# Kernel tuning notes

Measured on AMD Instinct MI355X. Metric: run time of the kernel, lower is better.

## Reference

```python
import jax, jax.numpy as jnp
import numpy as np
from jax import lax

NDF = 128
OUT_CH = 256
N_INPUT = 4096
H = W = 64
A_FEAT = OUT_CH * 2 * 2   # 1024
B_OUT = OUT_CH            # 256
C_ROW = 16
BATCH = 128
EPS = 1e-5


def conv2d_s2(x, w):
    # x: NCHW, w: OIHW, stride 2, pad 1 (kernel 4) -> halves spatial dims
    return lax.conv_general_dilated(x, w, window_strides=(2, 2),
                                    padding=[(1, 1), (1, 1)],
                                    dimension_numbers=("NCHW", "OIHW", "NCHW"))


def batchnorm(x, gamma, beta):
    # training-mode batch stats over (N, H, W)
    mean = jnp.mean(x, axis=(0, 2, 3), keepdims=True)
    var = jnp.var(x, axis=(0, 2, 3), keepdims=True)
    xn = (x - mean) * lax.rsqrt(var + EPS)
    return xn * gamma[None, :, None, None] + beta[None, :, None, None]


def lrelu(x):
    return jnp.where(x >= 0, x, 0.2 * x)


def setup_inputs() -> dict:
    key = jax.random.key(0)
    ks = jax.random.split(key, 16)
    s = lambda fan: 1.0 / np.sqrt(fan)
    inp = {
        "image": jax.random.normal(ks[0], (BATCH, 3, H, W), jnp.float32),
        "word_vectors": jax.random.normal(ks[1], (BATCH, N_INPUT), jnp.float32),
        "fc_w": jax.random.normal(ks[2], (H * W, N_INPUT), jnp.float32) * s(N_INPUT),
        "w1": jax.random.normal(ks[3], (NDF, 4, 4, 4), jnp.float32) * s(4 * 16),
        "w2": jax.random.normal(ks[4], (NDF * 2, NDF, 4, 4), jnp.float32) * s(NDF * 16),
        "w3": jax.random.normal(ks[5], (NDF * 2, NDF * 2, 4, 4), jnp.float32) * s(NDF * 2 * 16),
        "w4": jax.random.normal(ks[6], (NDF * 4, NDF * 2, 4, 4), jnp.float32) * s(NDF * 2 * 16),
        "w5": jax.random.normal(ks[7], (OUT_CH, NDF * 4, 4, 4), jnp.float32) * s(NDF * 4 * 16),
        "g2": jnp.ones((NDF * 2,), jnp.float32),
        "b2": jnp.zeros((NDF * 2,), jnp.float32),
        "g3": jnp.ones((NDF * 2,), jnp.float32),
        "b3": jnp.zeros((NDF * 2,), jnp.float32),
        "g4": jnp.ones((NDF * 4,), jnp.float32),
        "b4": jnp.zeros((NDF * 4,), jnp.float32),
        "T": jax.random.uniform(ks[8], (A_FEAT, B_OUT, C_ROW), jnp.float32,
                                 minval=0.0, maxval=1.0 / A_FEAT),
    }
    return inp


def reference(image, word_vectors, fc_w, w1, w2, w3, w4, w5,
              g2, b2, g3, b3, g4, b4, T):
    b = image.shape[0]
    # fc: Linear(no bias) + ReLU (dropout = identity at p=0 / eval)
    wv = jax.nn.relu(word_vectors @ fc_w.T)            # [b, H*W]
    wv = wv.reshape(b, 1, H, W)
    x = jnp.concatenate([image, wv], axis=1)           # [b, 4, 64, 64]
    # conv stack (spectral norm acts on weights; raw weights used here)
    x = lrelu(conv2d_s2(x, w1))                        # [b, ndf, 32, 32]
    x = lrelu(batchnorm(conv2d_s2(x, w2), g2, b2))     # [b, 2ndf, 16, 16]
    x = lrelu(batchnorm(conv2d_s2(x, w3), g3, b3))     # [b, 2ndf, 8, 8]
    x = lrelu(batchnorm(conv2d_s2(x, w4), g4, b4))     # [b, 4ndf, 4, 4]
    x = conv2d_s2(x, w5)                               # [b, out_ch, 2, 2]
    # minibatch discrimination
    feat = x.reshape(b, A_FEAT)                        # [b, 1024]
    Ms = (feat @ T.reshape(A_FEAT, B_OUT * C_ROW)).reshape(b, B_OUT, C_ROW)
    # pairwise L1 over C, exp, sum over batch (including self, as in the loop)
    d = jnp.sum(jnp.abs(Ms[:, None, :, :] - Ms[None, :, :, :]), axis=-1)  # [b,b,B]
    mbd = jnp.sum(jnp.exp(-d), axis=1)                 # [b, B]
    return jnp.concatenate([feat, mbd], axis=1)        # [b, 1280]
```

## Files before the change

### kernel.cpp

```cpp
#include <hip/hip_runtime.h>
#include <cstddef>

#define BB 128

typedef unsigned short u16;
typedef __attribute__((ext_vector_type(8))) short short8;
typedef __attribute__((ext_vector_type(4))) short short4v;
typedef __attribute__((ext_vector_type(4))) float f32x4;

constexpr int ilog2c(int v){ return v<=1 ? 0 : 1+ilog2c(v>>1); }

__device__ __forceinline__ u16 f2b(float f){
  union {float f; unsigned u;} x; x.f = f;
  unsigned u = x.u + 0x7fffu + ((x.u>>16)&1u);
  return (u16)(u>>16);
}
__device__ __forceinline__ float b2f(u16 h){
  union {unsigned u; float f;} x; x.u = ((unsigned)h)<<16;
  return x.f;
}

#define GLOAD_LDS16(gsrc, ldsdst) \
  __builtin_amdgcn_global_load_lds((const __attribute__((address_space(1))) void*)(gsrc), \
      (__attribute__((address_space(3))) void*)(ldsdst), 16, 0, 0)

template<int IC, int OC, int OH, int STORE, int KSPLIT=1>
__global__ __launch_bounds__(512) void convmm2(
    const u16* __restrict__ xp, const u16* __restrict__ wtT, void* __restrict__ yv)
{
  constexpr int OW = OH, S = OH*OW;
  constexpr int IHp = 2*OH+2, IWp = 2*OW+2;
  constexpr int KT = 16*IC;
  constexpr int KTS = KT / KSPLIT;
  constexpr int NT = KTS / 64;
  constexpr int LS = ilog2c(S), LOW = ilog2c(OW), L4 = ilog2c(4*IC);
  __shared__ u16 As[2*128*64];
  __shared__ u16 Bs[2*128*64];
  const int tid = threadIdx.x;
  const int m0 = blockIdx.x*128;
  const int n0 = blockIdx.y*128;
  const int kbase = (KSPLIT>1) ? blockIdx.z*KTS : 0;
  const int wave = tid>>6, l = tid&63;
  const int wm = wave>>1, wn = wave&1;

  size_t abase[2]; int au[2];
  #pragma unroll
  for (int t=0;t<2;++t){
    int unit = tid + t*512;
    int r = unit>>3, us = unit&7;
    au[t] = us ^ (r&7);
    int p = m0 + r;
    int b = p >> LS, s = p & (S-1);
    int oh = s >> LOW, ow = s & (OW-1);
    abase[t] = ((size_t)(b*IHp + 2*oh)*IWp + 2*ow)*IC;
  }
  const u16* bsrc[2];
  #pragma unroll
  for (int t=0;t<2;++t){
    int unit = tid + t*512;
    int r = unit>>3, us = unit&7;
    bsrc[t] = wtT + (size_t)(n0+r)*KT + (size_t)(us ^ (r&7))*8;
  }

  auto stage = [&](int half, int k0){
    #pragma unroll
    for (int t=0;t<2;++t){
      int k = k0 + au[t]*8;
      int kh = k >> L4, koff = k & (4*IC-1);
      GLOAD_LDS16(xp + abase[t] + (size_t)kh*IWp*IC + koff,
                  &As[half*8192 + (size_t)(t*512 + wave*64)*8]);
    }
    #pragma unroll
    for (int t=0;t<2;++t){
      GLOAD_LDS16(bsrc[t] + k0, &Bs[half*8192 + (size_t)(t*512 + wave*64)*8]);
    }
  };

  f32x4 acc[2][4] = {};

  stage(0, kbase);
  __syncthreads();
  int cur = 0;
  for (int t=0; t<NT; ++t){
    if (t+1 < NT) stage(cur^1, kbase + (t+1)*64);
    #pragma unroll
    for (int kk=0;kk<2;++kk){
      short8 af[2], bfm[4];
      #pragma unroll
      for (int mi=0;mi<2;++mi){
        int row = wm*32 + mi*16 + (l&15);
        int u = (kk*4 + (l>>4)) ^ (row&7);
        af[mi] = *(const short8*)(&As[cur*8192 + row*64 + u*8]);
      }
      #pragma unroll
      for (int ni=0;ni<4;++ni){
        int row = wn*64 + ni*16 + (l&15);
        int u = (kk*4 + (l>>4)) ^ (row&7);
        bfm[ni] = *(const short8*)(&Bs[cur*8192 + row*64 + u*8]);
      }
      #pragma unroll
      for (int mi=0;mi<2;++mi)
        #pragma unroll
        for (int ni=0;ni<4;++ni)
          acc[mi][ni] = __builtin_amdgcn_mfma_f32_16x16x32_bf16(af[mi], bfm[ni], acc[mi][ni], 0,0,0);
    }
    __syncthreads();
    cur ^= 1;
  }
  #pragma unroll
  for (int mi=0;mi<2;++mi){
    #pragma unroll
    for (int ni=0;ni<4;++ni){
      #pragma unroll
      for (int r=0;r<4;++r){
        int row = m0 + wm*32 + mi*16 + (l>>4)*4 + r;
        int col = n0 + wn*64 + ni*16 + (l&15);
        float v = acc[mi][ni][r];
        if (STORE==0){
          ((u16*)yv)[(size_t)row*OC + col] = f2b(v);
        } else if (STORE==1){
          v = v>=0.f ? v : 0.2f*v;
          int b = row>>LS, s = row&(S-1);
          int oh = s>>LOW, ow = s&(OW-1);
          ((u16*)yv)[((size_t)(b*(OH+2) + oh+1)*(OW+2) + ow+1)*OC + col] = f2b(v);
        } else {
          ((float*)yv)[((size_t)blockIdx.z*(BB*S) + row)*OC + col] = v;
        }
      }
    }
  }
}

template<int B_FP32>
__global__ __launch_bounds__(256) void gemm128_split(
    const u16* __restrict__ A, const void* __restrict__ Bsrc,
    float* __restrict__ part, int K, int kchunk)
{
  __shared__ u16 As[2*128*64];
  __shared__ u16 Bs[2*64*64];
  const int tid = threadIdx.x;
  const int n0 = blockIdx.x*64;
  const int kbase = blockIdx.y*kchunk;
  const int wave = tid>>6, l = tid&63;
  const u16* asrc[4];
  #pragma unroll
  for (int t=0;t<4;++t){
    int unit = tid + t*256, r = unit>>3, us = unit&7;
    asrc[t] = A + (size_t)r*K + (size_t)(us ^ (r&7))*8;
  }
  const float* bf32[4]; int bdst32[4];
  const u16* b16[2];
  if (B_FP32){
    const float* Bf = (const float*)Bsrc;
    #pragma unroll
    for (int t=0;t<4;++t){
      int unit = tid + t*256;
      int r = unit>>4, u4 = unit&15;
      int u = u4>>1, hf = u4&1;
      int us = u ^ (r&7);
      bf32[t] = Bf + (size_t)(n0+r)*K + u4*4;
      bdst32[t] = r*64 + us*8 + hf*4;
    }
  } else {
    const u16* Bb = (const u16*)Bsrc;
    #pragma unroll
    for (int t=0;t<2;++t){
      int unit = tid + t*256, r = unit>>3, us = unit&7;
      b16[t] = Bb + (size_t)(n0+r)*K + (size_t)(us ^ (r&7))*8;
    }
  }

  auto stageA = [&](int half, int k0){
    #pragma unroll
    for (int t=0;t<4;++t)
      GLOAD_LDS16(asrc[t] + k0, &As[half*8192 + (size_t)(t*256 + wave*64)*8]);
  };
  auto stageB16 = [&](int half, int k0){
    #pragma unroll
    for (int t=0;t<2;++t)
      GLOAD_LDS16(b16[t] + k0, &Bs[half*4096 + (size_t)(t*256 + wave*64)*8]);
  };
  float4 breg[4];
  auto loadB32 = [&](int k0){
    #pragma unroll
    for (int t=0;t<4;++t) breg[t] = *(const float4*)(bf32[t] + k0);
  };
  auto writeB32 = [&](int half){
    #pragma unroll
    for (int t=0;t<4;++t){
      short4v o; o[0]=(short)f2b(breg[t].x); o[1]=(short)f2b(breg[t].y);
      o[2]=(short)f2b(breg[t].z); o[3]=(short)f2b(breg[t].w);
      *(short4v*)(&Bs[half*4096 + bdst32[t]]) = o;
    }
  };

  f32x4 acc[2][4] = {};
  const int NT = kchunk >> 6;
  stageA(0, kbase);
  if (B_FP32){ loadB32(kbase); writeB32(0); } else stageB16(0, kbase);
  __syncthreads();
  int cur = 0;
  for (int t=0;t<NT;++t){
    const int k0 = kbase + t*64;
    if (t+1 < NT){
      stageA(cur^1, k0+64);
      if (B_FP32) loadB32(k0+64);
      else stageB16(cur^1, k0+64);
    }
    #pragma unroll
    for (int kk=0;kk<2;++kk){
      short8 af[2], bfm[4];
      #pragma unroll
      for (int mi=0;mi<2;++mi){
        int row = wave*32 + mi*16 + (l&15);
        int u = (kk*4 + (l>>4)) ^ (row&7);
        af[mi] = *(const short8*)(&As[cur*8192 + row*64 + u*8]);
      }
      #pragma unroll
      for (int ni=0;ni<4;++ni){
        int row = ni*16 + (l&15);
        int u = (kk*4 + (l>>4)) ^ (row&7);
        bfm[ni] = *(const short8*)(&Bs[cur*4096 + row*64 + u*8]);
      }
      #pragma unroll
      for (int mi=0;mi<2;++mi)
        #pragma unroll
        for (int ni=0;ni<4;++ni)
          acc[mi][ni] = __builtin_amdgcn_mfma_f32_16x16x32_bf16(af[mi], bfm[ni], acc[mi][ni], 0,0,0);
    }
    if (B_FP32 && t+1 < NT) writeB32(cur^1);
    __syncthreads();
    cur ^= 1;
  }
  #pragma unroll
  for (int mi=0;mi<2;++mi){
    #pragma unroll
    for (int ni=0;ni<4;++ni){
      #pragma unroll
      for (int r=0;r<4;++r){
        int m = wave*32 + mi*16 + (l>>4)*4 + r;
        int n = n0 + ni*16 + (l&15);
        part[((size_t)blockIdx.y*128 + m)*4096 + n] = acc[mi][ni][r];
      }
    }
  }
}

template<int NS, int STORE>
__global__ __launch_bounds__(256) void reduce_split(const float* __restrict__ part, void* __restrict__ outv)
{
  int idx = blockIdx.x*256 + threadIdx.x;
  float s = 0.f;
  #pragma unroll
  for (int i=0;i<NS;++i) s += part[(size_t)i*524288 + idx];
  if (STORE==0){
    float v = fmaxf(s, 0.f);
    int m = idx>>12, n = idx&4095;
    int h = n>>6, w2 = n&63;
    ((u16*)outv)[((size_t)(m*66 + h+1)*66 + w2+1)*8 + 3] = f2b(v);
  } else {
    ((float*)outv)[idx] = s;
  }
}

template<int NS, int C>
__global__ __launch_bounds__(256) void reduce_bn(
    const float* __restrict__ part, u16* __restrict__ y,
    float* __restrict__ stats, int Mblk, int Mtot)
{
  constexpr int CU = C/8, NR = 256/CU, LCU = ilog2c(CU);
  __shared__ float red[NR*C];
  const int cu = threadIdx.x & (CU-1);
  const int rg = threadIdx.x >> LCU;
  const int base = blockIdx.x*Mblk;
  float s[8] = {}, ss[8] = {};
  for (int p = base+rg; p < base+Mblk; p += NR){
    float a8[8];
    #pragma unroll
    for (int j=0;j<8;++j) a8[j]=0.f;
    #pragma unroll
    for (int i=0;i<NS;++i){
      const float* src = part + ((size_t)i*Mtot + p)*C + cu*8;
      float4 v0 = *(const float4*)src;
      float4 v1 = *(const float4*)(src+4);
      a8[0]+=v0.x; a8[1]+=v0.y; a8[2]+=v0.z; a8[3]+=v0.w;
      a8[4]+=v1.x; a8[5]+=v1.y; a8[6]+=v1.z; a8[7]+=v1.w;
    }
    u16 o[8];
    #pragma unroll
    for (int j=0;j<8;++j){
      o[j] = f2b(a8[j]);
      float vb = b2f(o[j]);
      s[j]+=vb; ss[j]+=vb*vb;
    }
    *(short8*)(y + (size_t)p*C + cu*8) = *(short8*)o;
  }
  #pragma unroll
  for (int j=0;j<8;++j) red[rg*C + cu*8 + j] = s[j];
  __syncthreads();
  for (int c=threadIdx.x; c<C; c+=256){
    float t=0.f;
    #pragma unroll
    for (int r2=0;r2<NR;++r2) t += red[r2*C+c];
    stats[blockIdx.x*512 + c] = t;
  }
  __syncthreads();
  #pragma unroll
  for (int j=0;j<8;++j) red[rg*C + cu*8 + j] = ss[j];
  __syncthreads();
  for (int c=threadIdx.x; c<C; c+=256){
    float t=0.f;
    #pragma unroll
    for (int r2=0;r2<NR;++r2) t += red[r2*C+c];
    stats[131072 + blockIdx.x*512 + c] = t;
  }
}

__global__ __launch_bounds__(256) void conv5_reduce(const float* __restrict__ part,
                                                    float* __restrict__ out, u16* __restrict__ featb)
{
  int idx = blockIdx.x*256 + threadIdx.x;
  float s = 0.f;
  #pragma unroll
  for (int i=0;i<32;++i) s += part[(size_t)i*131072 + idx];
  int row = idx>>8, col = idx&255;
  int b = row>>2, sp = row&3;
  out[(size_t)b*1280 + col*4 + sp] = s;
  featb[(size_t)b*1024 + col*4 + sp] = f2b(s);
}

template<int IC, int ICP>
__device__ __forceinline__ void repack_dev(const float* __restrict__ w, u16* __restrict__ wt,
                                           int oc, int tid, float* ls){
  for (int i=tid; i<IC*16; i+=256){
    int ic = i>>4, khkw = i&15;
    ls[ic*17+khkw] = w[(size_t)oc*IC*16 + i];
  }
  __syncthreads();
  constexpr int KT = 16*ICP;
  constexpr int LP = ilog2c(ICP);
  for (int k=tid; k<KT; k+=256){
    int khkw = k >> LP, ic = k & (ICP-1);
    float v = (ic<IC) ? ls[ic*17+khkw] : 0.f;
    wt[(size_t)oc*KT + k] = f2b(v);
  }
}

__device__ __forceinline__ void transpose_dev(const float* __restrict__ T, u16* __restrict__ Tt,
                                              int idx, int tid, float* tile){
  int bx = idx & 127, by = idx >> 7;
  int kb = by*32, nb = bx*32;
  int tx = tid&31, ty = tid>>5;
  #pragma unroll
  for (int i=0;i<32;i+=8)
    tile[(ty+i)*33 + tx] = T[(size_t)(kb+ty+i)*4096 + nb+tx];
  __syncthreads();
  #pragma unroll
  for (int i=0;i<32;i+=8)
    Tt[(size_t)(nb+ty+i)*1024 + kb+tx] = f2b(tile[tx*33 + ty+i]);
}

__global__ __launch_bounds__(256) void prep_all(
    const float* __restrict__ w1, const float* __restrict__ w2, const float* __restrict__ w3,
    const float* __restrict__ w4, const float* __restrict__ w5, const float* __restrict__ T,
    const float* __restrict__ wvec,
    u16* wt1T, u16* wt2T, u16* wt3T, u16* wt4T, u16* wt5T, u16* Tt, u16* wvb)
{
  __shared__ float ls[512*17];
  const int blk = blockIdx.x, tid = threadIdx.x;
  if (blk < 128)        repack_dev<4,8>(w1, wt1T, blk, tid, ls);
  else if (blk < 384)   repack_dev<128,128>(w2, wt2T, blk-128, tid, ls);
  else if (blk < 640)   repack_dev<256,256>(w3, wt3T, blk-384, tid, ls);
  else if (blk < 1152)  repack_dev<256,256>(w4, wt4T, blk-640, tid, ls);
  else if (blk < 1408)  repack_dev<512,512>(w5, wt5T, blk-1152, tid, ls);
  else if (blk < 5504)  transpose_dev(T, Tt, blk-1408, tid, ls);
  else { int i = (blk-5504)*256 + tid; wvb[i] = f2b(wvec[i]); }
}

template<int Hp, int C>
__device__ __forceinline__ void zb_border(u16* __restrict__ buf, int idx, int count){
  if (idx >= count) return;
  constexpr int NP = 4*Hp - 4;
  constexpr int PC = NP*C;
  int b = idx / PC;
  int rem = idx - b*PC;
  int p = rem >> ilog2c(C);
  int c = rem & (C-1);
  int h, w;
  if (p < Hp){ h = 0; w = p; }
  else if (p < 2*Hp){ h = Hp-1; w = p - Hp; }
  else { int q = p - 2*Hp; h = 1 + (q>>1); w = (q&1) ? (Hp-1) : 0; }
  buf[(((size_t)b*Hp + h)*Hp + w)*C + c] = 0;
}

__global__ __launch_bounds__(256) void zb_early(u16* xp0, u16* xp1, u16* xp2){
  const int blk = blockIdx.x, tid = threadIdx.x;
  if (blk < 1040)       zb_border<66,8>(xp0, blk*256 + tid, 266240);
  else if (blk < 9488)  zb_border<34,128>(xp1, (blk-1040)*256 + tid, 2162688);
  else                  zb_border<18,256>(xp2, (blk-9488)*256 + tid, 2228224);
}

__global__ __launch_bounds__(256) void zb_late(u16* xp3, u16* xp4){
  const int blk = blockIdx.x, tid = threadIdx.x;
  if (blk < 4608) zb_border<10,256>(xp3, blk*256 + tid, 1179648);
  else            zb_border<6,512>(xp4, (blk-4608)*256 + tid, 1310720);
}

__global__ __launch_bounds__(256) void pack_x0(const float* __restrict__ img, u16* __restrict__ xp0){
  int idx = blockIdx.x*256+threadIdx.x;
  int b = idx>>12, s = idx&4095;
  int h = s>>6, w = s&63;
  short8 o = {};
  o[0] = (short)f2b(img[(size_t)(b*3+0)*4096 + s]);
  o[1] = (short)f2b(img[(size_t)(b*3+1)*4096 + s]);
  o[2] = (short)f2b(img[(size_t)(b*3+2)*4096 + s]);
  *(short8*)(xp0 + ((size_t)(b*66 + h+1)*66 + w+1)*8) = o;
}

template<int C>
__global__ __launch_bounds__(256) void bn_stats2(const u16* __restrict__ y, float* __restrict__ stats, int Mblk){
  constexpr int CU = C/8, NR = 256/CU, LCU = ilog2c(CU);
  __shared__ float red[NR*C];
  const int cu = threadIdx.x & (CU-1);
  const int rg = threadIdx.x >> LCU;
  const int base = blockIdx.x*Mblk;
  float s[8] = {}, ss[8] = {};
  for (int p = base+rg; p < base+Mblk; p += NR){
    short8 v = *(const short8*)(y + (size_t)p*C + cu*8);
    #pragma unroll
    for (int j=0;j<8;++j){ float f=b2f((u16)v[j]); s[j]+=f; ss[j]+=f*f; }
  }
  #pragma unroll
  for (int j=0;j<8;++j) red[rg*C + cu*8 + j] = s[j];
  __syncthreads();
  for (int c=threadIdx.x; c<C; c+=256){
    float t=0.f;
    #pragma unroll
    for (int r2=0;r2<NR;++r2) t += red[r2*C+c];
    stats[blockIdx.x*512 + c] = t;
  }
  __syncthreads();
  #pragma unroll
  for (int j=0;j<8;++j) red[rg*C + cu*8 + j] = ss[j];
  __syncthreads();
  for (int c=threadIdx.x; c<C; c+=256){
    float t=0.f;
    #pragma unroll
    for (int r2=0;r2<NR;++r2) t += red[r2*C+c];
    stats[131072 + blockIdx.x*512 + c] = t;
  }
}

template<int C>
__global__ __launch_bounds__(C) void bn_finalize(float* __restrict__ stats, const float* __restrict__ g,
                                                 const float* __restrict__ be, float cnt){
  int c = threadIdx.x;
  float s=0.f, ss=0.f;
  for (int b=0;b<256;++b){ s += stats[b*512+c]; ss += stats[131072 + b*512+c]; }
  float m = s/cnt;
  float var = ss/cnt - m*m;
  float A = rsqrtf(var + 1e-5f)*g[c];
  stats[262144 + c] = A;
  stats[262144 + 512 + c] = be[c] - m*A;
}

template<int C, int OH>
__global__ __launch_bounds__(256) void bn_apply(const u16* __restrict__ y, const float* __restrict__ stats,
                                                u16* __restrict__ xp){
  constexpr int S = OH*OH, LS = ilog2c(S), LOW = ilog2c(OH);
  constexpr int CU = C/8, LCU = ilog2c(CU);
  int idx = blockIdx.x*256 + threadIdx.x;
  int p = idx >> LCU, cu = idx & (CU-1);
  short8 v8 = *(const short8*)(y + (size_t)p*C + cu*8);
  const float* Ap = stats + 262144;
  const float* Bp = stats + 262144 + 512;
  u16 o[8];
  #pragma unroll
  for (int j=0;j<8;++j){
    float v = b2f((u16)v8[j])*Ap[cu*8+j] + Bp[cu*8+j];
    o[j] = f2b(v>=0.f ? v : 0.2f*v);
  }
  int b = p>>LS, s = p&(S-1), oh = s>>LOW, ow = s&(OH-1);
  *(short8*)(xp + ((size_t)(b*(OH+2)+oh+1)*(OH+2)+ow+1)*C + cu*8) = *(short8*)o;
}

__global__ __launch_bounds__(256) void mbd_part(const float* __restrict__ Ms, float* __restrict__ part)
{
  const int i = blockIdx.x;
  const int ch = blockIdx.y;
  const int o = threadIdx.x;
  float mi[16];
  #pragma unroll
  for (int u = 0; u < 4; ++u) {
    float4 v = *(const float4*)&Ms[(size_t)i * 4096 + o * 16 + u * 4];
    mi[u*4+0]=v.x; mi[u*4+1]=v.y; mi[u*4+2]=v.z; mi[u*4+3]=v.w;
  }
  float acc = 0.f;
  for (int j = ch*16; j < ch*16 + 16; ++j) {
    float d = 0.f;
    #pragma unroll
    for (int u = 0; u < 4; ++u) {
      float4 v = *(const float4*)&Ms[(size_t)j * 4096 + o * 16 + u * 4];
      d += fabsf(mi[u*4+0]-v.x) + fabsf(mi[u*4+1]-v.y) + fabsf(mi[u*4+2]-v.z) + fabsf(mi[u*4+3]-v.w);
    }
    acc += __expf(-d);
  }
  part[((size_t)ch*128 + i)*256 + o] = acc;
}

__global__ __launch_bounds__(256) void mbd_reduce(const float* __restrict__ part, float* __restrict__ out)
{
  int idx = blockIdx.x*256 + threadIdx.x;
  int i = idx>>8, o = idx&255;
  float s = 0.f;
  #pragma unroll
  for (int c=0;c<8;++c) s += part[((size_t)c*128 + i)*256 + o];
  out[(size_t)i*1280 + 1024 + o] = s;
}

__global__ void ws_too_small(float* out, int n){
  int idx = blockIdx.x*256+threadIdx.x;
  if (idx<n) out[idx] = -777.0f;
}

extern "C" void kernel_launch(void* const* d_in, const int* in_sizes, int n_in,
                              void* d_out, int out_size, void* d_ws, size_t ws_size,
                              hipStream_t stream)
{
  const float* image = (const float*)d_in[0];
  const float* wvec  = (const float*)d_in[1];
  const float* fc_w  = (const float*)d_in[2];
  const float* w1    = (const float*)d_in[3];
  const float* w2    = (const float*)d_in[4];
  const float* w3    = (const float*)d_in[5];
  const float* w4    = (const float*)d_in[6];
  const float* w5    = (const float*)d_in[7];
  const float* g2    = (const float*)d_in[8];
  const float* b2    = (const float*)d_in[9];
  const float* g3    = (const float*)d_in[10];
  const float* b3    = (const float*)d_in[11];
  const float* g4    = (const float*)d_in[12];
  const float* b4    = (const float*)d_in[13];
  const float* T     = (const float*)d_in[14];
  float* out = (float*)d_out;
  char* wsb = (char*)d_ws;

  const size_t NEED = 105816064ull;
  if (ws_size < NEED) {
    ws_too_small<<<(out_size + 255)/256, 256, 0, stream>>>(out, out_size);
    return;
  }

  u16* xp1   = (u16*)(wsb + 0);
  u16* y3    = (u16*)(wsb + 0);
  u16* xp3   = (u16*)(wsb + 4194304);
  u16* y4    = (u16*)(wsb + 10747904);
  u16* xp4   = (u16*)(wsb + 12845056);
  float* Ms  = (float*)(wsb + 17563648);
  u16* featb = (u16*)(wsb + 19660800);
  float* stats = (float*)(wsb + 19922944);
  u16* xp2   = (u16*)(wsb + 37879808);
  float* c4part = (float*)(wsb + 37879808);
  float* c5part = (float*)(wsb + 37879808);
  float* mbdpart = (float*)(wsb + 37879808);
  u16* y2    = (u16*)(wsb + 59113472);
  float* gpart  = (float*)(wsb + 59113472);
  float* c3part = (float*)(wsb + 59113472);
  u16* xp0   = (u16*)(wsb + 75890688);
  u16* wt1T  = (u16*)(wsb + 84811776);
  u16* wt2T  = (u16*)(wsb + 84844544);
  u16* wt3T  = (u16*)(wsb + 85893120);
  u16* wt4T  = (u16*)(wsb + 87990272);
  u16* wt5T  = (u16*)(wsb + 92184576);
  u16* Tt    = (u16*)(wsb + 96378880);
  u16* wvb   = (u16*)(wsb + 104767488);

  prep_all<<<7552, 256, 0, stream>>>(w1, w2, w3, w4, w5, T, wvec,
                                     wt1T, wt2T, wt3T, wt4T, wt5T, Tt, wvb);
  pack_x0<<<2048, 256, 0, stream>>>(image, xp0);
  zb_early<<<18192, 256, 0, stream>>>(xp0, xp1, xp2);

  gemm128_split<1><<<dim3(64,8), 256, 0, stream>>>(wvb, fc_w, gpart, 4096, 512);
  reduce_split<8,0><<<2048, 256, 0, stream>>>(gpart, xp0);

  convmm2<8,128,32,1><<<dim3(1024,1), 512, 0, stream>>>(xp0, wt1T, xp1);
  convmm2<128,256,16,0><<<dim3(256,2), 512, 0, stream>>>(xp1, wt2T, y2);

  zb_late<<<9728, 256, 0, stream>>>(xp3, xp4);

  bn_stats2<256><<<256, 256, 0, stream>>>(y2, stats, 128);
  bn_finalize<256><<<1, 256, 0, stream>>>(stats, g2, b2, 32768.f);
  bn_apply<256,16><<<4096, 256, 0, stream>>>(y2, stats, xp2);

  convmm2<256,256,8,3,2><<<dim3(64,2,2), 512, 0, stream>>>(xp2, wt3T, c3part);
  reduce_bn<2,256><<<256, 256, 0, stream>>>(c3part, y3, stats, 32, 8192);
  bn_finalize<256><<<1, 256, 0, stream>>>(stats, g3, b3, 8192.f);
  bn_apply<256,8><<<1024, 256, 0, stream>>>(y3, stats, xp3);

  convmm2<256,512,4,3,4><<<dim3(16,4,4), 512, 0, stream>>>(xp3, wt4T, c4part);
  reduce_bn<4,512><<<256, 256, 0, stream>>>(c4part, y4, stats, 8, 2048);
  bn_finalize<512><<<1, 512, 0, stream>>>(stats, g4, b4, 2048.f);
  bn_apply<512,4><<<512, 256, 0, stream>>>(y4, stats, xp4);

  convmm2<512,256,2,3,32><<<dim3(4,2,32), 512, 0, stream>>>(xp4, wt5T, c5part);
  conv5_reduce<<<512, 256, 0, stream>>>(c5part, out, featb);

  gemm128_split<0><<<dim3(64,8), 256, 0, stream>>>(featb, Tt, gpart, 1024, 128);
  reduce_split<8,1><<<2048, 256, 0, stream>>>(gpart, Ms);

  mbd_part<<<dim3(128,8), 256, 0, stream>>>(Ms, mbdpart);
  mbd_reduce<<<128, 256, 0, stream>>>(mbdpart, out);
}
```

Measured before the change: 269.5 us.

## Fuse prep/pack/border kernels, shrink conv1 channel padding, deepen FC split-K

Folds image packing and xp0 border zeroing into the prep kernel. Merges the FC split-K reduction with the xp1/xp2 border zeroing, and the bn_apply for layer 2 with the xp3/xp4 border zeroing, which removes several launches. Conv1 input channels are padded to 4 instead of 8, halving xp0 traffic and conv1 K work. The FC GEMM split-K goes from 8 to 16 slices (K chunk 256) with a separate partial buffer, which adds more parallelism at the cost of more partial-sum traffic.

Result: no change. 266.9 us (-1.0%).

```diff
diff --git a/kernel.cpp b/kernel.cpp
--- a/kernel.cpp
+++ b/kernel.cpp
@@ -246,137 +246,6 @@
   }
 }
 
-template<int NS, int STORE>
-__global__ __launch_bounds__(256) void reduce_split(const float* __restrict__ part, void* __restrict__ outv)
-{
-  int idx = blockIdx.x*256 + threadIdx.x;
-  float s = 0.f;
-  #pragma unroll
-  for (int i=0;i<NS;++i) s += part[(size_t)i*524288 + idx];
-  if (STORE==0){
-    float v = fmaxf(s, 0.f);
-    int m = idx>>12, n = idx&4095;
-    int h = n>>6, w2 = n&63;
-    ((u16*)outv)[((size_t)(m*66 + h+1)*66 + w2+1)*8 + 3] = f2b(v);
-  } else {
-    ((float*)outv)[idx] = s;
-  }
-}
-
-template<int NS, int C>
-__global__ __launch_bounds__(256) void reduce_bn(
-    const float* __restrict__ part, u16* __restrict__ y,
-    float* __restrict__ stats, int Mblk, int Mtot)
-{
-  constexpr int CU = C/8, NR = 256/CU, LCU = ilog2c(CU);
-  __shared__ float red[NR*C];
-  const int cu = threadIdx.x & (CU-1);
-  const int rg = threadIdx.x >> LCU;
-  const int base = blockIdx.x*Mblk;
-  float s[8] = {}, ss[8] = {};
-  for (int p = base+rg; p < base+Mblk; p += NR){
-    float a8[8];
-    #pragma unroll
-    for (int j=0;j<8;++j) a8[j]=0.f;
-    #pragma unroll
-    for (int i=0;i<NS;++i){
-      const float* src = part + ((size_t)i*Mtot + p)*C + cu*8;
-      float4 v0 = *(const float4*)src;
-      float4 v1 = *(const float4*)(src+4);
-      a8[0]+=v0.x; a8[1]+=v0.y; a8[2]+=v0.z; a8[3]+=v0.w;
-      a8[4]+=v1.x; a8[5]+=v1.y; a8[6]+=v1.z; a8[7]+=v1.w;
-    }
-    u16 o[8];
-    #pragma unroll
-    for (int j=0;j<8;++j){
-      o[j] = f2b(a8[j]);
-      float vb = b2f(o[j]);
-      s[j]+=vb; ss[j]+=vb*vb;
-    }
-    *(short8*)(y + (size_t)p*C + cu*8) = *(short8*)o;
-  }
-  #pragma unroll
-  for (int j=0;j<8;++j) red[rg*C + cu*8 + j] = s[j];
-  __syncthreads();
-  for (int c=threadIdx.x; c<C; c+=256){
-    float t=0.f;
-    #pragma unroll
-    for (int r2=0;r2<NR;++r2) t += red[r2*C+c];
-    stats[blockIdx.x*512 + c] = t;
-  }
-  __syncthreads();
-  #pragma unroll
-  for (int j=0;j<8;++j) red[rg*C + cu*8 + j] = ss[j];
-  __syncthreads();
-  for (int c=threadIdx.x; c<C; c+=256){
-    float t=0.f;
-    #pragma unroll
-    for (int r2=0;r2<NR;++r2) t += red[r2*C+c];
-    stats[131072 + blockIdx.x*512 + c] = t;
-  }
-}
-
-__global__ __launch_bounds__(256) void conv5_reduce(const float* __restrict__ part,
-                                                    float* __restrict__ out, u16* __restrict__ featb)
-{
-  int idx = blockIdx.x*256 + threadIdx.x;
-  float s = 0.f;
-  #pragma unroll
-  for (int i=0;i<32;++i) s += part[(size_t)i*131072 + idx];
-  int row = idx>>8, col = idx&255;
-  int b = row>>2, sp = row&3;
-  out[(size_t)b*1280 + col*4 + sp] = s;
-  featb[(size_t)b*1024 + col*4 + sp] = f2b(s);
-}
-
-template<int IC, int ICP>
-__device__ __forceinline__ void repack_dev(const float* __restrict__ w, u16* __restrict__ wt,
-                                           int oc, int tid, float* ls){
-  for (int i=tid; i<IC*16; i+=256){
-    int ic = i>>4, khkw = i&15;
-    ls[ic*17+khkw] = w[(size_t)oc*IC*16 + i];
-  }
-  __syncthreads();
-  constexpr int KT = 16*ICP;
-  constexpr int LP = ilog2c(ICP);
-  for (int k=tid; k<KT; k+=256){
-    int khkw = k >> LP, ic = k & (ICP-1);
-    float v = (ic<IC) ? ls[ic*17+khkw] : 0.f;
-    wt[(size_t)oc*KT + k] = f2b(v);
-  }
-}
-
-__device__ __forceinline__ void transpose_dev(const float* __restrict__ T, u16* __restrict__ Tt,
-                                              int idx, int tid, float* tile){
-  int bx = idx & 127, by = idx >> 7;
-  int kb = by*32, nb = bx*32;
-  int tx = tid&31, ty = tid>>5;
-  #pragma unroll
-  for (int i=0;i<32;i+=8)
-    tile[(ty+i)*33 + tx] = T[(size_t)(kb+ty+i)*4096 + nb+tx];
-  __syncthreads();
-  #pragma unroll
-  for (int i=0;i<32;i+=8)
-    Tt[(size_t)(nb+ty+i)*1024 + kb+tx] = f2b(tile[tx*33 + ty+i]);
-}
-
-__global__ __launch_bounds__(256) void prep_all(
-    const float* __restrict__ w1, const float* __restrict__ w2, const float* __restrict__ w3,
-    const float* __restrict__ w4, const float* __restrict__ w5, const float* __restrict__ T,
-    const float* __restrict__ wvec,
-    u16* wt1T, u16* wt2T, u16* wt3T, u16* wt4T, u16* wt5T, u16* Tt, u16* wvb)
-{
-  __shared__ float ls[512*17];
-  const int blk = blockIdx.x, tid = threadIdx.x;
-  if (blk < 128)        repack_dev<4,8>(w1, wt1T, blk, tid, ls);
-  else if (blk < 384)   repack_dev<128,128>(w2, wt2T, blk-128, tid, ls);
-  else if (blk < 640)   repack_dev<256,256>(w3, wt3T, blk-384, tid, ls);
-  else if (blk < 1152)  repack_dev<256,256>(w4, wt4T, blk-640, tid, ls);
-  else if (blk < 1408)  repack_dev<512,512>(w5, wt5T, blk-1152, tid, ls);
-  else if (blk < 5504)  transpose_dev(T, Tt, blk-1408, tid, ls);
-  else { int i = (blk-5504)*256 + tid; wvb[i] = f2b(wvec[i]); }
-}
-
 template<int Hp, int C>
 __device__ __forceinline__ void zb_border(u16* __restrict__ buf, int idx, int count){
   if (idx >= count) return;
@@ -393,28 +262,161 @@
   buf[(((size_t)b*Hp + h)*Hp + w)*C + c] = 0;
 }
 
-__global__ __launch_bounds__(256) void zb_early(u16* xp0, u16* xp1, u16* xp2){
+__global__ __launch_bounds__(256) void fc_reduce_zb(const float* __restrict__ part,
+                                                    u16* __restrict__ xp0,
+                                                    u16* __restrict__ xp1, u16* __restrict__ xp2)
+{
   const int blk = blockIdx.x, tid = threadIdx.x;
-  if (blk < 1040)       zb_border<66,8>(xp0, blk*256 + tid, 266240);
-  else if (blk < 9488)  zb_border<34,128>(xp1, (blk-1040)*256 + tid, 2162688);
-  else                  zb_border<18,256>(xp2, (blk-9488)*256 + tid, 2228224);
-}
-
-__global__ __launch_bounds__(256) void zb_late(u16* xp3, u16* xp4){
+  if (blk < 2048){
+    int idx = blk*256 + tid;
+    float s = 0.f;
+    #pragma unroll
+    for (int i=0;i<16;++i) s += part[(size_t)i*524288 + idx];
+    float v = fmaxf(s, 0.f);
+    int m = idx>>12, n = idx&4095;
+    int h = n>>6, w2 = n&63;
+    xp0[((size_t)(m*66 + h+1)*66 + w2+1)*4 + 3] = f2b(v);
+  } else if (blk < 10496){
+    zb_border<34,128>(xp1, (blk-2048)*256 + tid, 2162688);
+  } else {
+    zb_border<18,256>(xp2, (blk-10496)*256 + tid, 2228224);
+  }
+}
+
+__global__ __launch_bounds__(256) void reduce_ms(const float* __restrict__ part, float* __restrict__ outv)
+{
+  int idx = blockIdx.x*256 + threadIdx.x;
+  float s = 0.f;
+  #pragma unroll
+  for (int i=0;i<8;++i) s += part[(size_t)i*524288 + idx];
+  outv[idx] = s;
+}
+
+template<int NS, int C>
+__global__ __launch_bounds__(256) void reduce_bn(
+    const float* __restrict__ part, u16* __restrict__ y,
+    float* __restrict__ stats, int Mblk, int Mtot)
+{
+  constexpr int CU = C/8, NR = 256/CU, LCU = ilog2c(CU);
+  __shared__ float red[NR*C];
+  const int cu = threadIdx.x & (CU-1);
+  const int rg = threadIdx.x >> LCU;
+  const int base = blockIdx.x*Mblk;
+  float s[8] = {}, ss[8] = {};
+  for (int p = base+rg; p < base+Mblk; p += NR){
+    float a8[8];
+    #pragma unroll
+    for (int j=0;j<8;++j) a8[j]=0.f;
+    #pragma unroll
+    for (int i=0;i<NS;++i){
+      const float* src = part + ((size_t)i*Mtot + p)*C + cu*8;
+      float4 v0 = *(const float4*)src;
+      float4 v1 = *(const float4*)(src+4);
+      a8[0]+=v0.x; a8[1]+=v0.y; a8[2]+=v0.z; a8[3]+=v0.w;
+      a8[4]+=v1.x; a8[5]+=v1.y; a8[6]+=v1.z; a8[7]+=v1.w;
+    }
+    u16 o[8];
+    #pragma unroll
+    for (int j=0;j<8;++j){
+      o[j] = f2b(a8[j]);
+      float vb = b2f(o[j]);
+      s[j]+=vb; ss[j]+=vb*vb;
+    }
+    *(short8*)(y + (size_t)p*C + cu*8) = *(short8*)o;
+  }
+  #pragma unroll
+  for (int j=0;j<8;++j) red[rg*C + cu*8 + j] = s[j];
+  __syncthreads();
+  for (int c=threadIdx.x; c<C; c+=256){
+    float t=0.f;
+    #pragma unroll
+    for (int r2=0;r2<NR;++r2) t += red[r2*C+c];
+    stats[blockIdx.x*512 + c] = t;
+  }
+  __syncthreads();
+  #pragma unroll
+  for (int j=0;j<8;++j) red[rg*C + cu*8 + j] = ss[j];
+  __syncthreads();
+  for (int c=threadIdx.x; c<C; c+=256){
+    float t=0.f;
+    #pragma unroll
+    for (int r2=0;r2<NR;++r2) t += red[r2*C+c];
+    stats[131072 + blockIdx.x*512 + c] = t;
+  }
+}
+
+__global__ __launch_bounds__(256) void conv5_reduce(const float* __restrict__ part,
+                                                    float* __restrict__ out, u16* __restrict__ featb)
+{
+  int idx = blockIdx.x*256 + threadIdx.x;
+  float s = 0.f;
+  #pragma unroll
+  for (int i=0;i<32;++i) s += part[(size_t)i*131072 + idx];
+  int row = idx>>8, col = idx&255;
+  int b = row>>2, sp = row&3;
+  out[(size_t)b*1280 + col*4 + sp] = s;
+  featb[(size_t)b*1024 + col*4 + sp] = f2b(s);
+}
+
+template<int IC, int ICP>
+__device__ __forceinline__ void repack_dev(const float* __restrict__ w, u16* __restrict__ wt,
+                                           int oc, int tid, float* ls){
+  for (int i=tid; i<IC*16; i+=256){
+    int ic = i>>4, khkw = i&15;
+    ls[ic*17+khkw] = w[(size_t)oc*IC*16 + i];
+  }
+  __syncthreads();
+  constexpr int KT = 16*ICP;
+  constexpr int LP = ilog2c(ICP);
+  for (int k=tid; k<KT; k+=256){
+    int khkw = k >> LP, ic = k & (ICP-1);
+    float v = (ic<IC) ? ls[ic*17+khkw] : 0.f;
+    wt[(size_t)oc*KT + k] = f2b(v);
+  }
+}
+
+__device__ __forceinline__ void transpose_dev(const float* __restrict__ T, u16* __restrict__ Tt,
+                                              int idx, int tid, float* tile){
+  int bx = idx & 127, by = idx >> 7;
+  int kb = by*32, nb = bx*32;
+  int tx = tid&31, ty = tid>>5;
+  #pragma unroll
+  for (int i=0;i<32;i+=8)
+    tile[(ty+i)*33 + tx] = T[(size_t)(kb+ty+i)*4096 + nb+tx];
+  __syncthreads();
+  #pragma unroll
+  for (int i=0;i<32;i+=8)
+    Tt[(size_t)(nb+ty+i)*1024 + kb+tx] = f2b(tile[tx*33 + ty+i]);
+}
+
+__global__ __launch_bounds__(256) void prep_all(
+    const float* __restrict__ w1, const float* __restrict__ w2, const float* __restrict__ w3,
+    const float* __restrict__ w4, const float* __restrict__ w5, const float* __restrict__ T,
+    const float* __restrict__ wvec, const float* __restrict__ img,
+    u16* wt1T, u16* wt2T, u16* wt3T, u16* wt4T, u16* wt5T, u16* Tt, u16* wvb, u16* xp0)
+{
+  __shared__ float ls[512*17];
   const int blk = blockIdx.x, tid = threadIdx.x;
-  if (blk < 4608) zb_border<10,256>(xp3, blk*256 + tid, 1179648);
-  else            zb_border<6,512>(xp4, (blk-4608)*256 + tid, 1310720);
-}
-
-__global__ __launch_bounds__(256) void pack_x0(const float* __restrict__ img, u16* __restrict__ xp0){
-  int idx = blockIdx.x*256+threadIdx.x;
-  int b = idx>>12, s = idx&4095;
-  int h = s>>6, w = s&63;
-  short8 o = {};
-  o[0] = (short)f2b(img[(size_t)(b*3+0)*4096 + s]);
-  o[1] = (short)f2b(img[(size_t)(b*3+1)*4096 + s]);
-  o[2] = (short)f2b(img[(size_t)(b*3+2)*4096 + s]);
-  *(short8*)(xp0 + ((size_t)(b*66 + h+1)*66 + w+1)*8) = o;
+  if (blk < 128)        repack_dev<4,4>(w1, wt1T, blk, tid, ls);
+  else if (blk < 384)   repack_dev<128,128>(w2, wt2T, blk-128, tid, ls);
+  else if (blk < 640)   repack_dev<256,256>(w3, wt3T, blk-384, tid, ls);
+  else if (blk < 1152)  repack_dev<256,256>(w4, wt4T, blk-640, tid, ls);
+  else if (blk < 1408)  repack_dev<512,512>(w5, wt5T, blk-1152, tid, ls);
+  else if (blk < 5504)  transpose_dev(T, Tt, blk-1408, tid, ls);
+  else if (blk < 7552){ int i = (blk-5504)*256 + tid; wvb[i] = f2b(wvec[i]); }
+  else if (blk < 9600){
+    int idx = (blk-7552)*256 + tid;
+    int b = idx>>12, s = idx&4095;
+    int h = s>>6, w = s&63;
+    short4v o;
+    o[0] = (short)f2b(img[(size_t)(b*3+0)*4096 + s]);
+    o[1] = (short)f2b(img[(size_t)(b*3+1)*4096 + s]);
+    o[2] = (short)f2b(img[(size_t)(b*3+2)*4096 + s]);
+    o[3] = 0;
+    *(short4v*)(xp0 + ((size_t)(b*66 + h+1)*66 + w+1)*4) = o;
+  } else {
+    zb_border<66,4>(xp0, (blk-9600)*256 + tid, 133120);
+  }
 }
 
 template<int C>
@@ -465,11 +467,10 @@
 }
 
 template<int C, int OH>
-__global__ __launch_bounds__(256) void bn_apply(const u16* __restrict__ y, const float* __restrict__ stats,
-                                                u16* __restrict__ xp){
+__device__ __forceinline__ void bn_apply_body(const u16* __restrict__ y, const float* __restrict__ stats,
+                                              u16* __restrict__ xp, int idx){
   constexpr int S = OH*OH, LS = ilog2c(S), LOW = ilog2c(OH);
   constexpr int CU = C/8, LCU = ilog2c(CU);
-  int idx = blockIdx.x*256 + threadIdx.x;
   int p = idx >> LCU, cu = idx & (CU-1);
   short8 v8 = *(const short8*)(y + (size_t)p*C + cu*8);
   const float* Ap = stats + 262144;
@@ -482,6 +483,20 @@
   }
   int b = p>>LS, s = p&(S-1), oh = s>>LOW, ow = s&(OH-1);
   *(short8*)(xp + ((size_t)(b*(OH+2)+oh+1)*(OH+2)+ow+1)*C + cu*8) = *(short8*)o;
+}
+
+template<int C, int OH>
+__global__ __launch_bounds__(256) void bn_apply(const u16* __restrict__ y, const float* __restrict__ stats,
+                                                u16* __restrict__ xp){
+  bn_apply_body<C,OH>(y, stats, xp, blockIdx.x*256 + threadIdx.x);
+}
+
+__global__ __launch_bounds__(256) void bn_apply2_zb(const u16* __restrict__ y, const float* __restrict__ stats,
+                                                    u16* __restrict__ xp, u16* xp3, u16* xp4){
+  const int blk = blockIdx.x, tid = threadIdx.x;
+  if (blk < 4096)       bn_apply_body<256,16>(y, stats, xp, blk*256 + tid);
+  else if (blk < 8704)  zb_border<10,256>(xp3, (blk-4096)*256 + tid, 1179648);
+  else                  zb_border<6,512>(xp4, (blk-8704)*256 + tid, 1310720);
 }
 
 __global__ __launch_bounds__(256) void mbd_part(const float* __restrict__ Ms, float* __restrict__ part)
@@ -560,11 +575,12 @@
   u16* featb = (u16*)(wsb + 19660800);
   float* stats = (float*)(wsb + 19922944);
   u16* xp2   = (u16*)(wsb + 37879808);
+  float* gpartF = (float*)(wsb + 37879808);
   float* c4part = (float*)(wsb + 37879808);
   float* c5part = (float*)(wsb + 37879808);
   float* mbdpart = (float*)(wsb + 37879808);
   u16* y2    = (u16*)(wsb + 59113472);
-  float* gpart  = (float*)(wsb + 59113472);
+  float* gpartM = (float*)(wsb + 59113472);
   float* c3part = (float*)(wsb + 59113472);
   u16* xp0   = (u16*)(wsb + 75890688);
   u16* wt1T  = (u16*)(wsb + 84811776);
@@ -575,22 +591,18 @@
   u16* Tt    = (u16*)(wsb + 96378880);
   u16* wvb   = (u16*)(wsb + 104767488);
 
-  prep_all<<<7552, 256, 0, stream>>>(w1, w2, w3, w4, w5, T, wvec,
-                                     wt1T, wt2T, wt3T, wt4T, wt5T, Tt, wvb);
-  pack_x0<<<2048, 256, 0, stream>>>(image, xp0);
-  zb_early<<<18192, 256, 0, stream>>>(xp0, xp1, xp2);
-
-  gemm128_split<1><<<dim3(64,8), 256, 0, stream>>>(wvb, fc_w, gpart, 4096, 512);
-  reduce_split<8,0><<<2048, 256, 0, stream>>>(gpart, xp0);
-
-  convmm2<8,128,32,1><<<dim3(1024,1), 512, 0, stream>>>(xp0, wt1T, xp1);
+  prep_all<<<10120, 256, 0, stream>>>(w1, w2, w3, w4, w5, T, wvec, image,
+                                      wt1T, wt2T, wt3T, wt4T, wt5T, Tt, wvb, xp0);
+
+  gemm128_split<1><<<dim3(64,16), 256, 0, stream>>>(wvb, fc_w, gpartF, 4096, 256);
+  fc_reduce_zb<<<19200, 256, 0, stream>>>(gpartF, xp0, xp1, xp2);
+
+  convmm2<4,128,32,1><<<dim3(1024,1), 512, 0, stream>>>(xp0, wt1T, xp1);
   convmm2<128,256,16,0><<<dim3(256,2), 512, 0, stream>>>(xp1, wt2T, y2);
-
-  zb_late<<<9728, 256, 0, stream>>>(xp3, xp4);
 
   bn_stats2<256><<<256, 256, 0, stream>>>(y2, stats, 128);
   bn_finalize<256><<<1, 256, 0, stream>>>(stats, g2, b2, 32768.f);
-  bn_apply<256,16><<<4096, 256, 0, stream>>>(y2, stats, xp2);
+  bn_apply2_zb<<<13824, 256, 0, stream>>>(y2, stats, xp2, xp3, xp4);
 
   convmm2<256,256,8,3,2><<<dim3(64,2,2), 512, 0, stream>>>(xp2, wt3T, c3part);
   reduce_bn<2,256><<<256, 256, 0, stream>>>(c3part, y3, stats, 32, 8192);
@@ -605,8 +617,8 @@
   convmm2<512,256,2,3,32><<<dim3(4,2,32), 512, 0, stream>>>(xp4, wt5T, c5part);
   conv5_reduce<<<512, 256, 0, stream>>>(c5part, out, featb);
 
-  gemm128_split<0><<<dim3(64,8), 256, 0, stream>>>(featb, Tt, gpart, 1024, 128);
-  reduce_split<8,1><<<2048, 256, 0, stream>>>(gpart, Ms);
+  gemm128_split<0><<<dim3(64,8), 256, 0, stream>>>(featb, Tt, gpartM, 1024, 128);
+  reduce_ms<<<2048, 256, 0, stream>>>(gpartM, Ms);
 
   mbd_part<<<dim3(128,8), 256, 0, stream>>>(Ms, mbdpart);
   mbd_reduce<<<128, 256, 0, stream>>>(mbdpart, out);
```
